# Performance work log

Hardware: AMD Instinct MI355X
Metric: run time of the kernel (lower is better)

Reference implementation:

```python
import jax, jax.numpy as jnp
import numpy as np

N_NODES = 100000
N_EDGES = 1000000
D = 64
N_GRAPHS = 128
N_LAYERS = 3
BN_EPS = 1e-5


def setup_inputs() -> dict:
    key = jax.random.key(0)
    ks = jax.random.split(key, 8)
    x = jax.random.normal(ks[0], (N_NODES, D), dtype=jnp.float32)
    edge_index = jax.random.randint(ks[1], (2, N_EDGES), 0, N_NODES, dtype=jnp.int64)
    edge_attr = jax.random.uniform(ks[2], (N_EDGES,), dtype=jnp.float32)
    batch = jnp.sort(jax.random.randint(ks[3], (N_NODES,), 0, N_GRAPHS, dtype=jnp.int64))
    # xavier-uniform linear weights [L, out, in], zero conv bias (PyG GCNConv adds bias after aggregation)
    limit = float(np.sqrt(6.0 / (D + D)))
    W = jax.random.uniform(ks[4], (N_LAYERS, D, D), minval=-limit, maxval=limit, dtype=jnp.float32)
    b = jnp.zeros((N_LAYERS, D), dtype=jnp.float32)
    prelu_a = jnp.asarray(0.25, dtype=jnp.float32)  # single PReLU shared across layers
    bn_w = jnp.ones((N_LAYERS, D), dtype=jnp.float32)
    bn_b = jnp.zeros((N_LAYERS, D), dtype=jnp.float32)
    return {"x": x, "edge_index": edge_index, "edge_attr": edge_attr, "batch": batch,
            "W": W, "b": b, "prelu_a": prelu_a, "bn_w": bn_w, "bn_b": bn_b}


def reference(x, edge_index, edge_attr, batch, W, b, prelu_a, bn_w, bn_b):
    src, dst = edge_index[0], edge_index[1]
    h = x
    pooled = []
    for i in range(N_LAYERS):
        # GCNConv (normalize=False, add_self_loops=False): lin -> weighted scatter-add -> bias
        h = h @ W[i].T                                      # [N, D]
        msg = h[src] * edge_attr[:, None]                   # [E, D] gather + scale
        h = jax.ops.segment_sum(msg, dst, num_segments=N_NODES) + b[i]
        # shared PReLU
        h = jnp.where(h >= 0, h, prelu_a * h)
        # BatchNorm1d (training mode: biased batch stats over nodes)
        mean = jnp.mean(h, axis=0)
        var = jnp.mean((h - mean) ** 2, axis=0)
        h = (h - mean) * jax.lax.rsqrt(var + BN_EPS) * bn_w[i] + bn_b[i]
        pooled.append(jax.ops.segment_sum(h, batch, num_segments=N_GRAPHS))
    global_rep = jnp.concatenate(pooled, axis=1)            # [G, L*D]
    x_stack = pooled[-1]                                    # [G, D]
    return (global_rep, x_stack)
```

## Files before the change

### kernel.cpp

```cpp
#include <hip/hip_runtime.h>

#define NNODES 100000
#define NEDGES 1000000
#define DIM 64
#define NGRAPHS 128
#define NLAYERS 3
#define BN_EPS 1e-5f

#define BINSZ 8
#define NBINS 12500
#define GBLK 256
#define ECHUNK 3907
#define SLICES 4

#define OFF_EDGES   0
#define OFF_BINBASE 2000000
#define OFF_AGG     2012544
#define OFF_YBF     8412544
#define OFF_XBF     11612544
#define OFF_CNT     14812544
#define OFF_OFS     16412544
#define OFF_BTOT    18012544
#define OFF_GSUM4   18025088
#define OFF_PQ4     18057856
#define OFF_SCALE   18090624
#define OFF_SHIFT   18090816
#define OFF_END     18091008

__device__ __forceinline__ unsigned pack_bf16(float a, float b) {
    unsigned ua = __float_as_uint(a), ub = __float_as_uint(b);
    ua = (ua + 0x7FFFu + ((ua >> 16) & 1u)) >> 16;
    ub = (ub + 0x7FFFu + ((ub >> 16) & 1u)) & 0xFFFF0000u;
    return ua | ub;
}
__device__ __forceinline__ float bflo(unsigned u) { return __uint_as_float(u << 16); }
__device__ __forceinline__ float bfhi(unsigned u) { return __uint_as_float(u & 0xFFFF0000u); }

__global__ __launch_bounds__(1024) void count_kernel(const int* __restrict__ ei,
                                                     const float* __restrict__ x,
                                                     const int* __restrict__ batch,
                                                     unsigned short* __restrict__ counts,
                                                     unsigned* __restrict__ xbf,
                                                     int* __restrict__ endv) {
    __shared__ int hist[NBINS];
    const int tid = threadIdx.x, blk = blockIdx.x;
    for (int i = tid; i < NBINS; i += 1024) hist[i] = 0;
    __syncthreads();
    const int e0 = blk * ECHUNK, e1 = min(NEDGES, e0 + ECHUNK);
    for (int e = e0 + tid; e < e1; e += 1024)
        atomicAdd(&hist[ei[NEDGES + e] >> 3], 1);
    __syncthreads();
    unsigned short* crow = counts + (size_t)blk * NBINS;
    for (int bin = tid; bin < NBINS; bin += 1024)
        crow[bin] = (unsigned short)hist[bin];
    const int gtid = blk * 1024 + tid;
    for (int i = gtid; i < NNODES * 32; i += GBLK * 1024) {
        const float2 v = *(const float2*)(x + (size_t)i * 2);
        xbf[i] = pack_bf16(v.x, v.y);
    }
    for (int i = gtid; i < NNODES; i += GBLK * 1024) {
        const int b0 = batch[i];
        const int b1 = (i + 1 < NNODES) ? batch[i + 1] : NGRAPHS;
        for (int g = b0; g < b1; ++g) endv[g] = i + 1;
        if (i == 0)
            for (int g = 0; g < b0; ++g) endv[g] = 0;
    }
}

__global__ __launch_bounds__(256) void s1_kernel(const unsigned short* __restrict__ counts,
                                                 unsigned short* __restrict__ offs,
                                                 int* __restrict__ btot) {
    const int bin = blockIdx.x * 256 + threadIdx.x;
    if (bin >= NBINS) return;
    int run = 0;
    for (int blk = 0; blk < GBLK; ++blk) {
        const int v = counts[(size_t)blk * NBINS + bin];
        offs[(size_t)blk * NBINS + bin] = (unsigned short)run;
        run += v;
    }
    btot[bin] = run;
}

__global__ __launch_bounds__(1024) void s2_kernel(const int* __restrict__ btot,
                                                  int* __restrict__ binBase) {
    __shared__ int wsum[16];
    const int t = threadIdx.x, wid = t >> 6, lane = t & 63;
    int running = 0;
    for (int b = 0; b < NBINS; b += 1024) {
        const int i = b + t;
        const int v = (i < NBINS) ? btot[i] : 0;
        int s = v;
        for (int off = 1; off < 64; off <<= 1) {
            int x = __shfl_up(s, off);
            if (lane >= off) s += x;
        }
        __syncthreads();
        if (lane == 63) wsum[wid] = s;
        __syncthreads();
        int pw = 0, tot = 0;
#pragma unroll
        for (int k = 0; k < 16; ++k) {
            const int x = wsum[k];
            tot += x;
            if (k < wid) pw += x;
        }
        if (i < NBINS) binBase[i] = running + pw + s - v;
        running += tot;
    }
    if (t == 0) binBase[NBINS] = running;
}

__global__ __launch_bounds__(1024) void scatter_kernel(const int* __restrict__ ei,
                                                       const float* __restrict__ ea,
                                                       const int* __restrict__ binBase,
                                                       const unsigned short* __restrict__ offs,
                                                       int2* __restrict__ edges) {
    __shared__ int cur[NBINS];
    const int tid = threadIdx.x, blk = blockIdx.x;
    const unsigned short* orow = offs + (size_t)blk * NBINS;
    for (int i = tid; i < NBINS; i += 1024)
        cur[i] = binBase[i] + (int)orow[i];
    __syncthreads();
    const int e0 = blk * ECHUNK, e1 = min(NEDGES, e0 + ECHUNK);
    for (int e = e0 + tid; e < e1; e += 1024) {
        const int dst = ei[NEDGES + e];
        const int src = ei[e];
        const float w = ea[e];
        const int pos = atomicAdd(&cur[dst >> 3], 1);
        edges[pos] = make_int2((src << 3) | (dst & (BINSZ - 1)), __float_as_int(w));
    }
}

template <bool FIRST>
__global__ __launch_bounds__(256) void agg_kernel(const unsigned* __restrict__ hbf,
                                                  const float* __restrict__ scale,
                                                  const float* __restrict__ shift,
                                                  const int* __restrict__ binBase,
                                                  const int2* __restrict__ edges,
                                                  unsigned* __restrict__ aggbf) {
    __shared__ float accAll[4][2][BINSZ * 64];
    const int w = threadIdx.x >> 6, lane = threadIdx.x & 63;
    const int bin = blockIdx.x * 4 + w;
    const int half = lane >> 5, p = lane & 31, c0 = 2 * p;
    float* ac = accAll[w][half];
#pragma unroll
    for (int r = 0; r < BINSZ; ++r) *(float2*)&ac[r * 64 + c0] = make_float2(0.f, 0.f);
    float sc0 = 1.f, sc1 = 1.f, sh0 = 0.f, sh1 = 0.f;
    if (!FIRST) { sc0 = scale[c0]; sc1 = scale[c0 + 1]; sh0 = shift[c0]; sh1 = shift[c0 + 1]; }
    const int beg = binBase[bin], end = binBase[bin + 1];
    for (int j = beg; j < end; j += 64) {
        const int n = min(64, end - j);
        int2 ed = (j + lane < end) ? edges[j + lane] : make_int2(0, 0);
        const int n16 = n & ~15;
        int t = 0;
        for (; t < n16; t += 16) {
            int sd_[8]; float wt_[8]; unsigned u_[8];
#pragma unroll
            for (int q = 0; q < 8; ++q) {
                const int ii = t + 2 * q + half;
                sd_[q] = __shfl(ed.x, ii);
                wt_[q] = __int_as_float(__shfl(ed.y, ii));
            }
#pragma unroll
            for (int q = 0; q < 8; ++q) u_[q] = hbf[(size_t)(sd_[q] >> 3) * 32 + p];
#pragma unroll
            for (int q = 0; q < 8; ++q) {
                float h0 = bflo(u_[q]);
                float h1 = bfhi(u_[q]);
                if (!FIRST) { h0 = fmaf(h0, sc0, sh0); h1 = fmaf(h1, sc1, sh1); }
                float2* a2 = (float2*)&ac[(sd_[q] & 7) * 64 + c0];
                float2 v = *a2;
                v.x = fmaf(wt_[q], h0, v.x);
                v.y = fmaf(wt_[q], h1, v.y);
                *a2 = v;
            }
        }
        for (; t < n; t += 2) {
            const int ii = min(t + half, n - 1);
            const int sd = __shfl(ed.x, ii);
            float wt = __int_as_float(__shfl(ed.y, ii));
            if (t + half >= n) wt = 0.f;
            const unsigned u = hbf[(size_t)(sd >> 3) * 32 + p];
            float h0 = bflo(u);
            float h1 = bfhi(u);
            if (!FIRST) { h0 = fmaf(h0, sc0, sh0); h1 = fmaf(h1, sc1, sh1); }
            float2* a2 = (float2*)&ac[(sd & 7) * 64 + c0];
            float2 v = *a2;
            v.x = fmaf(wt, h0, v.x);
            v.y = fmaf(wt, h1, v.y);
            *a2 = v;
        }
    }
    const int nodeBase = bin * BINSZ;
#pragma unroll
    for (int i = 0; i < 4; ++i) {
        const int idx = lane + 64 * i;
        const int r = idx >> 5, p2 = idx & 31;
        const float2 a0 = *(const float2*)&accAll[w][0][r * 64 + 2 * p2];
        const float2 a1 = *(const float2*)&accAll[w][1][r * 64 + 2 * p2];
        aggbf[(size_t)(nodeBase + r) * 32 + p2] = pack_bf16(a0.x + a1.x, a0.y + a1.y);
    }
}

__global__ __launch_bounds__(256) void gemm_kernel(const unsigned* __restrict__ aggbf,
                                                   const float* __restrict__ W,
                                                   const float* __restrict__ bias,
                                                   const float* __restrict__ pa_ptr,
                                                   unsigned* __restrict__ ybf) {
    __shared__ float As[128 * 68];
    __shared__ float Wt[64 * 68];
    const int tid = threadIdx.x;
    const int base = blockIdx.x * 128;
    for (int i = tid; i < 2048; i += 256) {
        const int r = i >> 4;
        const int q = i & 15;
        const int row = base + r;
        float4 v = make_float4(0.f, 0.f, 0.f, 0.f);
        if (row < NNODES) {
            const uint2 u = *(const uint2*)&aggbf[(size_t)row * 32 + q * 2];
            v = make_float4(bflo(u.x), bfhi(u.x), bflo(u.y), bfhi(u.y));
        }
        *(float4*)&As[r * 68 + q * 4] = v;
    }
    for (int i = tid; i < 4096; i += 256)
        Wt[(i & 63) * 68 + (i >> 6)] = W[i];
    __syncthreads();

    const int tc = tid & 7;
    const int tr = tid >> 3;
    float acc[4][8];
#pragma unroll
    for (int j = 0; j < 4; ++j)
#pragma unroll
        for (int c = 0; c < 8; ++c) acc[j][c] = 0.f;

    for (int kc = 0; kc < 16; ++kc) {
        const int k0 = kc * 4;
        float Af[4][4];
#pragma unroll
        for (int j = 0; j < 4; ++j) {
            const float4 t = *(const float4*)&As[(tr + 32 * j) * 68 + k0];
            Af[j][0] = t.x; Af[j][1] = t.y; Af[j][2] = t.z; Af[j][3] = t.w;
        }
#pragma unroll
        for (int kk = 0; kk < 4; ++kk) {
            const float4 w0 = *(const float4*)&Wt[(k0 + kk) * 68 + tc * 8];
            const float4 w1 = *(const float4*)&Wt[(k0 + kk) * 68 + tc * 8 + 4];
#pragma unroll
            for (int j = 0; j < 4; ++j) {
                const float a = Af[j][kk];
                acc[j][0] = fmaf(a, w0.x, acc[j][0]);
                acc[j][1] = fmaf(a, w0.y, acc[j][1]);
                acc[j][2] = fmaf(a, w0.z, acc[j][2]);
                acc[j][3] = fmaf(a, w0.w, acc[j][3]);
                acc[j][4] = fmaf(a, w1.x, acc[j][4]);
                acc[j][5] = fmaf(a, w1.y, acc[j][5]);
                acc[j][6] = fmaf(a, w1.z, acc[j][6]);
                acc[j][7] = fmaf(a, w1.w, acc[j][7]);
            }
        }
    }

    const float pa = *pa_ptr;
    const float4 b0 = *(const float4*)(bias + tc * 8);
    const float4 b1 = *(const float4*)(bias + tc * 8 + 4);
#pragma unroll
    for (int j = 0; j < 4; ++j) {
        const int row = base + tr + 32 * j;
        if (row >= NNODES) continue;
        float o[8];
        o[0] = acc[j][0] + b0.x; o[1] = acc[j][1] + b0.y;
        o[2] = acc[j][2] + b0.z; o[3] = acc[j][3] + b0.w;
        o[4] = acc[j][4] + b1.x; o[5] = acc[j][5] + b1.y;
        o[6] = acc[j][6] + b1.z; o[7] = acc[j][7] + b1.w;
#pragma unroll
        for (int c = 0; c < 8; ++c) o[c] = (o[c] >= 0.f) ? o[c] : pa * o[c];
        uint4 pk;
        pk.x = pack_bf16(o[0], o[1]);
        pk.y = pack_bf16(o[2], o[3]);
        pk.z = pack_bf16(o[4], o[5]);
        pk.w = pack_bf16(o[6], o[7]);
        *(uint4*)(ybf + (size_t)row * 32 + tc * 4) = pk;
    }
}

__global__ __launch_bounds__(256) void stats_kernel(const unsigned* __restrict__ ybf,
                                                    const int* __restrict__ endv,
                                                    float* __restrict__ gsum4,
                                                    float* __restrict__ pQ4) {
    __shared__ float red[2][32][66];
    const int g = blockIdx.x >> 2, s = blockIdx.x & 3;
    const int t = threadIdx.x, rg = t >> 3, cg = t & 7;
    const int g0 = (g == 0) ? 0 : endv[g - 1];
    const int g1 = endv[g];
    const int len = g1 - g0;
    const int q0 = g0 + (len * s) / SLICES;
    const int q1 = g0 + (len * (s + 1)) / SLICES;
    float sm[8], sq[8];
#pragma unroll
    for (int k = 0; k < 8; ++k) { sm[k] = 0.f; sq[k] = 0.f; }
    for (int r = q0 + rg; r < q1; r += 32) {
        const uint4 u4 = *(const uint4*)&ybf[(size_t)r * 32 + cg * 4];
        const unsigned uu[4] = {u4.x, u4.y, u4.z, u4.w};
#pragma unroll
        for (int k = 0; k < 4; ++k) {
            const float f0 = bflo(uu[k]);
            const float f1 = bfhi(uu[k]);
            sm[2 * k] += f0; sm[2 * k + 1] += f1;
            sq[2 * k] = fmaf(f0, f0, sq[2 * k]);
            sq[2 * k + 1] = fmaf(f1, f1, sq[2 * k + 1]);
        }
    }
#pragma unroll
    for (int k = 0; k < 8; ++k) {
        red[0][rg][cg * 8 + k] = sm[k];
        red[1][rg][cg * 8 + k] = sq[k];
    }
    __syncthreads();
    if (t < 128) {
        const int which = t >> 6, c = t & 63;
        float a = 0.f;
#pragma unroll
        for (int k = 0; k < 32; ++k) a += red[which][k][c];
        if (which == 0) gsum4[blockIdx.x * 64 + c] = a;
        else            pQ4[blockIdx.x * 64 + c] = a;
    }
}

__global__ __launch_bounds__(512) void finalize_kernel(const float* __restrict__ gsum4,
                                                       const float* __restrict__ pQ4,
                                                       const int* __restrict__ endv,
                                                       const float* __restrict__ bn_w,
                                                       const float* __restrict__ bn_b,
                                                       float* __restrict__ scale,
                                                       float* __restrict__ shift,
                                                       float* __restrict__ out, int layer) {
    __shared__ float rS[8][64], rQ[8][64];
    __shared__ float ssc[64], ssh[64];
    const int tid = threadIdx.x;
    const int c = tid & 63, pp = tid >> 6;
    float S = 0.f, Q = 0.f;
    for (int sl = pp; sl < NGRAPHS * SLICES; sl += 8) {
        S += gsum4[sl * 64 + c];
        Q += pQ4[sl * 64 + c];
    }
    rS[pp][c] = S; rQ[pp][c] = Q;
    __syncthreads();
    if (tid < 64) {
        float SS = 0.f, QQ = 0.f;
#pragma unroll
        for (int k = 0; k < 8; ++k) { SS += rS[k][c]; QQ += rQ[k][c]; }
        const float mean = SS * (1.f / NNODES);
        const float var = fmaxf(QQ * (1.f / NNODES) - mean * mean, 0.f);
        const float inv = rsqrtf(var + BN_EPS);
        const float scv = inv * bn_w[c];
        const float shv = bn_b[c] - mean * scv;
        ssc[c] = scv; ssh[c] = shv;
        scale[c] = scv; shift[c] = shv;
    }
    __syncthreads();
    for (int idx = tid; idx < NGRAPHS * 64; idx += 512) {
        const int g = idx >> 6, ch = idx & 63;
        float gs = 0.f;
#pragma unroll
        for (int sl = 0; sl < SLICES; ++sl) gs += gsum4[(g * SLICES + sl) * 64 + ch];
        const int cnt = endv[g] - ((g == 0) ? 0 : endv[g - 1]);
        const float pooled = gs * ssc[ch] + (float)cnt * ssh[ch];
        out[g * (NLAYERS * 64) + layer * 64 + ch] = pooled;
        if (layer == NLAYERS - 1) out[NGRAPHS * NLAYERS * 64 + idx] = pooled;
    }
}

extern "C" void kernel_launch(void* const* d_in, const int* in_sizes, int n_in,
                              void* d_out, int out_size, void* d_ws, size_t ws_size,
                              hipStream_t stream) {
    const float* x     = (const float*)d_in[0];
    const int*   ei    = (const int*)d_in[1];
    const float* ea    = (const float*)d_in[2];
    const int*   batch = (const int*)d_in[3];
    const float* W     = (const float*)d_in[4];
    const float* b     = (const float*)d_in[5];
    const float* pa    = (const float*)d_in[6];
    const float* bn_w  = (const float*)d_in[7];
    const float* bn_b  = (const float*)d_in[8];
    float* out = (float*)d_out;
    float* ws  = (float*)d_ws;
    int*   wsi = (int*)d_ws;

    int2*           edges   = (int2*)(wsi + OFF_EDGES);
    int*            binBase = wsi + OFF_BINBASE;
    unsigned*       aggbf   = (unsigned*)(wsi + OFF_AGG);
    unsigned*       ybf     = (unsigned*)(wsi + OFF_YBF);
    unsigned*       xbf     = (unsigned*)(wsi + OFF_XBF);
    unsigned short* counts  = (unsigned short*)(wsi + OFF_CNT);
    unsigned short* offs    = (unsigned short*)(wsi + OFF_OFS);
    int*            btot    = wsi + OFF_BTOT;
    float*          gsum4   = ws + OFF_GSUM4;
    float*          pQ4     = ws + OFF_PQ4;
    float*          scaleA  = ws + OFF_SCALE;
    float*          shiftA  = ws + OFF_SHIFT;
    int*            endv    = wsi + OFF_END;

    count_kernel<<<GBLK, 1024, 0, stream>>>(ei, x, batch, counts, xbf, endv);
    s1_kernel<<<(NBINS + 255) / 256, 256, 0, stream>>>(counts, offs, btot);
    s2_kernel<<<1, 1024, 0, stream>>>(btot, binBase);
    scatter_kernel<<<GBLK, 1024, 0, stream>>>(ei, ea, binBase, offs, edges);

    for (int l = 0; l < NLAYERS; ++l) {
        if (l == 0)
            agg_kernel<true><<<NBINS / 4, 256, 0, stream>>>(xbf, nullptr, nullptr,
                                                            binBase, edges, aggbf);
        else
            agg_kernel<false><<<NBINS / 4, 256, 0, stream>>>(ybf, scaleA + (l - 1) * 64,
                                                             shiftA + (l - 1) * 64,
                                                             binBase, edges, aggbf);
        gemm_kernel<<<(NNODES + 127) / 128, 256, 0, stream>>>(aggbf, W + l * 4096,
                                                              b + l * 64, pa, ybf);
        stats_kernel<<<NGRAPHS * SLICES, 256, 0, stream>>>(ybf, endv, gsum4, pQ4);
        finalize_kernel<<<1, 512, 0, stream>>>(gsum4, pQ4, endv, bn_w + l * 64,
                                               bn_b + l * 64, scaleA + l * 64,
                                               shiftA + l * 64, out, l);
    }
}
```

Before: 297.3 us.

## Move BN affine out of edge aggregation using precomputed weighted in-degree

Rather than applying the previous layer's BatchNorm scale and shift to every gathered edge message, aggregation now sums the raw bf16 features. The gemm prologue applies scale to the aggregate and adds shift times the node's weighted in-degree, which a new one-time wdeg kernel computes. This removes two FMAs per edge element in the hot aggregation loop, at the cost of an extra kernel pass over the edges and a per-row wdeg load. The x-to-bf16 conversion is also widened to float4 loads.

Measured after the change: 305.1 us. 1.03x slower.

```diff
diff --git a/kernel.cpp b/kernel.cpp
--- a/kernel.cpp
+++ b/kernel.cpp
@@ -26,6 +26,7 @@
 #define OFF_SCALE   18090624
 #define OFF_SHIFT   18090816
 #define OFF_END     18091008
+#define OFF_WDEG    18091136
 
 __device__ __forceinline__ unsigned pack_bf16(float a, float b) {
     unsigned ua = __float_as_uint(a), ub = __float_as_uint(b);
@@ -54,9 +55,9 @@
     for (int bin = tid; bin < NBINS; bin += 1024)
         crow[bin] = (unsigned short)hist[bin];
     const int gtid = blk * 1024 + tid;
-    for (int i = gtid; i < NNODES * 32; i += GBLK * 1024) {
-        const float2 v = *(const float2*)(x + (size_t)i * 2);
-        xbf[i] = pack_bf16(v.x, v.y);
+    for (int i = gtid; i < NNODES * 16; i += GBLK * 1024) {
+        const float4 v = *(const float4*)(x + (size_t)i * 4);
+        *(uint2*)&xbf[(size_t)i * 2] = make_uint2(pack_bf16(v.x, v.y), pack_bf16(v.z, v.w));
     }
     for (int i = gtid; i < NNODES; i += GBLK * 1024) {
         const int b0 = batch[i];
@@ -131,10 +132,28 @@
     }
 }
 
-template <bool FIRST>
+__global__ __launch_bounds__(256) void wdeg_kernel(const int* __restrict__ binBase,
+                                                   const int2* __restrict__ edges,
+                                                   float* __restrict__ wdeg) {
+    __shared__ float lwd[4][64 * 9];
+    const int w = threadIdx.x >> 6, lane = threadIdx.x & 63;
+    const int bin = blockIdx.x * 4 + w;
+    float* L = lwd[w];
+#pragma unroll
+    for (int r = 0; r < 9; ++r) L[lane * 9 + r] = 0.f;
+    const int beg = binBase[bin], end = binBase[bin + 1];
+    for (int j = beg + lane; j < end; j += 64) {
+        const int2 e = edges[j];
+        L[lane * 9 + (e.x & 7)] += __int_as_float(e.y);
+    }
+    if (lane < 8) {
+        float s = 0.f;
+        for (int l = 0; l < 64; ++l) s += L[l * 9 + lane];
+        wdeg[bin * BINSZ + lane] = s;
+    }
+}
+
 __global__ __launch_bounds__(256) void agg_kernel(const unsigned* __restrict__ hbf,
-                                                  const float* __restrict__ scale,
-                                                  const float* __restrict__ shift,
                                                   const int* __restrict__ binBase,
                                                   const int2* __restrict__ edges,
                                                   unsigned* __restrict__ aggbf) {
@@ -145,8 +164,6 @@
     float* ac = accAll[w][half];
 #pragma unroll
     for (int r = 0; r < BINSZ; ++r) *(float2*)&ac[r * 64 + c0] = make_float2(0.f, 0.f);
-    float sc0 = 1.f, sc1 = 1.f, sh0 = 0.f, sh1 = 0.f;
-    if (!FIRST) { sc0 = scale[c0]; sc1 = scale[c0 + 1]; sh0 = shift[c0]; sh1 = shift[c0 + 1]; }
     const int beg = binBase[bin], end = binBase[bin + 1];
     for (int j = beg; j < end; j += 64) {
         const int n = min(64, end - j);
@@ -165,13 +182,10 @@
             for (int q = 0; q < 8; ++q) u_[q] = hbf[(size_t)(sd_[q] >> 3) * 32 + p];
 #pragma unroll
             for (int q = 0; q < 8; ++q) {
-                float h0 = bflo(u_[q]);
-                float h1 = bfhi(u_[q]);
-                if (!FIRST) { h0 = fmaf(h0, sc0, sh0); h1 = fmaf(h1, sc1, sh1); }
                 float2* a2 = (float2*)&ac[(sd_[q] & 7) * 64 + c0];
                 float2 v = *a2;
-                v.x = fmaf(wt_[q], h0, v.x);
-                v.y = fmaf(wt_[q], h1, v.y);
+                v.x = fmaf(wt_[q], bflo(u_[q]), v.x);
+                v.y = fmaf(wt_[q], bfhi(u_[q]), v.y);
                 *a2 = v;
             }
         }
@@ -181,13 +195,10 @@
             float wt = __int_as_float(__shfl(ed.y, ii));
             if (t + half >= n) wt = 0.f;
             const unsigned u = hbf[(size_t)(sd >> 3) * 32 + p];
-            float h0 = bflo(u);
-            float h1 = bfhi(u);
-            if (!FIRST) { h0 = fmaf(h0, sc0, sh0); h1 = fmaf(h1, sc1, sh1); }
             float2* a2 = (float2*)&ac[(sd & 7) * 64 + c0];
             float2 v = *a2;
-            v.x = fmaf(wt, h0, v.x);
-            v.y = fmaf(wt, h1, v.y);
+            v.x = fmaf(wt, bflo(u), v.x);
+            v.y = fmaf(wt, bfhi(u), v.y);
             *a2 = v;
         }
     }
@@ -202,7 +213,11 @@
     }
 }
 
+template <bool FIRST>
 __global__ __launch_bounds__(256) void gemm_kernel(const unsigned* __restrict__ aggbf,
+                                                   const float* __restrict__ scale,
+                                                   const float* __restrict__ shift,
+                                                   const float* __restrict__ wdeg,
                                                    const float* __restrict__ W,
                                                    const float* __restrict__ bias,
                                                    const float* __restrict__ pa_ptr,
@@ -218,7 +233,17 @@
         float4 v = make_float4(0.f, 0.f, 0.f, 0.f);
         if (row < NNODES) {
             const uint2 u = *(const uint2*)&aggbf[(size_t)row * 32 + q * 2];
-            v = make_float4(bflo(u.x), bfhi(u.x), bflo(u.y), bfhi(u.y));
+            if (FIRST) {
+                v = make_float4(bflo(u.x), bfhi(u.x), bflo(u.y), bfhi(u.y));
+            } else {
+                const float4 sc4 = *(const float4*)(scale + q * 4);
+                const float4 sh4 = *(const float4*)(shift + q * 4);
+                const float wd = wdeg[row];
+                v.x = fmaf(bflo(u.x), sc4.x, sh4.x * wd);
+                v.y = fmaf(bfhi(u.x), sc4.y, sh4.y * wd);
+                v.z = fmaf(bflo(u.y), sc4.z, sh4.z * wd);
+                v.w = fmaf(bfhi(u.y), sc4.w, sh4.w * wd);
+            }
         }
         *(float4*)&As[r * 68 + q * 4] = v;
     }
@@ -400,22 +425,24 @@
     float*          scaleA  = ws + OFF_SCALE;
     float*          shiftA  = ws + OFF_SHIFT;
     int*            endv    = wsi + OFF_END;
+    float*          wdeg    = ws + OFF_WDEG;
 
     count_kernel<<<GBLK, 1024, 0, stream>>>(ei, x, batch, counts, xbf, endv);
     s1_kernel<<<(NBINS + 255) / 256, 256, 0, stream>>>(counts, offs, btot);
     s2_kernel<<<1, 1024, 0, stream>>>(btot, binBase);
     scatter_kernel<<<GBLK, 1024, 0, stream>>>(ei, ea, binBase, offs, edges);
+    wdeg_kernel<<<NBINS / 4, 256, 0, stream>>>(binBase, edges, wdeg);
 
     for (int l = 0; l < NLAYERS; ++l) {
+        agg_kernel<<<NBINS / 4, 256, 0, stream>>>((l == 0) ? xbf : ybf,
+                                                  binBase, edges, aggbf);
         if (l == 0)
-            agg_kernel<true><<<NBINS / 4, 256, 0, stream>>>(xbf, nullptr, nullptr,
-                                                            binBase, edges, aggbf);
+            gemm_kernel<true><<<(NNODES + 127) / 128, 256, 0, stream>>>(
+                aggbf, nullptr, nullptr, wdeg, W, b, pa, ybf);
         else
-            agg_kernel<false><<<NBINS / 4, 256, 0, stream>>>(ybf, scaleA + (l - 1) * 64,
-                                                             shiftA + (l - 1) * 64,
-                                                             binBase, edges, aggbf);
-        gemm_kernel<<<(NNODES + 127) / 128, 256, 0, stream>>>(aggbf, W + l * 4096,
-                                                              b + l * 64, pa, ybf);
+            gemm_kernel<false><<<(NNODES + 127) / 128, 256, 0, stream>>>(
+                aggbf, scaleA + (l - 1) * 64, shiftA + (l - 1) * 64, wdeg,
+                W + l * 4096, b + l * 64, pa, ybf);
         stats_kernel<<<NGRAPHS * SLICES, 256, 0, stream>>>(ybf, endv, gsum4, pQ4);
         finalize_kernel<<<1, 512, 0, stream>>>(gsum4, pQ4, endv, bn_w + l * 64,
                                                bn_b + l * 64, scaleA + l * 64,
```
